# Kernel tuning notes

Measured on AMD Instinct MI355X. Metric: run time of the kernel, lower is better.

## Reference

```python
import jax, jax.numpy as jnp
import numpy as np

T, B, D = 256, 64, 512


def setup_inputs() -> dict:
    key = jax.random.key(0)
    ks = jax.random.split(key, 9)
    s = 1.0 / np.sqrt(D)  # torch Linear default init scale (uniform), use scaled normal
    return {
        "x": jax.random.normal(ks[0], (T, B, D), dtype=jnp.float32),
        "y": jax.random.normal(ks[1], (T, B, D), dtype=jnp.float32),
        "Wr": jax.random.normal(ks[2], (D, D), dtype=jnp.float32) * s,
        "Ur": jax.random.normal(ks[3], (D, D), dtype=jnp.float32) * s,
        "Wz": jax.random.normal(ks[4], (D, D), dtype=jnp.float32) * s,
        "Uz": jax.random.normal(ks[5], (D, D), dtype=jnp.float32) * s,
        "Wg": jax.random.normal(ks[6], (D, D), dtype=jnp.float32) * s,
        "Ug": jax.random.normal(ks[7], (D, D), dtype=jnp.float32) * s,
        "bg": jnp.full((D,), 2.0, dtype=jnp.float32),
    }


def reference(x, y, Wr, Ur, Wz, Uz, Wg, Ug, bg):
    # GTrXL gating unit. torch Linear(y) == y @ W.T
    r = jax.nn.sigmoid(jnp.einsum("tbd,ed->tbe", y, Wr) + jnp.einsum("tbd,ed->tbe", x, Ur))
    z = jax.nn.sigmoid(jnp.einsum("tbd,ed->tbe", y, Wz) + jnp.einsum("tbd,ed->tbe", x, Uz) - bg)
    h = jnp.tanh(jnp.einsum("tbd,ed->tbe", y, Wg) + jnp.einsum("tbd,ed->tbe", r * x, Ug))
    g = (1.0 - z) * x + z * h  # (T, B, D)
    return g
```

## Files before the change

kernel.cpp:

```cpp
#include <hip/hip_runtime.h>
#include <stdint.h>

typedef unsigned short u16;
typedef __attribute__((ext_vector_type(8))) __bf16 bf16x8;
typedef __attribute__((ext_vector_type(4))) float f32x4;

#define Tn 256
#define Bn 64
#define Dn 512
#define Mn (Tn * Bn)


__device__ __forceinline__ u16 f2bf(float f) {
  unsigned u = __float_as_uint(f);
  u += 0x7fffu + ((u >> 16) & 1u);
  return (u16)(u >> 16);
}

__device__ __forceinline__ float bf2f(u16 b) {
  return __uint_as_float(((unsigned)b) << 16);
}

__device__ __forceinline__ void async16(const u16* g, u16* l) {
  __builtin_amdgcn_global_load_lds(
      (const __attribute__((address_space(1))) unsigned int*)g,
      (__attribute__((address_space(3))) unsigned int*)l, 16, 0, 0);
}

__device__ __forceinline__ float sigmoidf_(float v) {
  return 1.f / (1.f + __expf(-v));
}

__global__ void cast_all(const float* __restrict__ y, const float* __restrict__ x,
                         const float* w0, const float* w1, const float* w2,
                         const float* w3, const float* w4, const float* w5,
                         u16* __restrict__ yb, u16* __restrict__ xb,
                         u16* __restrict__ wb) {
  int b = blockIdx.x;
  const float* src;
  u16* dst;
  if (b < 8192) {
    src = y; dst = yb;
  } else if (b < 16384) {
    src = x; dst = xb; b -= 8192;
  } else {
    b -= 16384;
    const int wi = b >> 8;
    b &= 255;
    src = wi == 0 ? w0 : wi == 1 ? w1 : wi == 2 ? w2 : wi == 3 ? w3 : wi == 4 ? w4 : w5;
    dst = wb + wi * 262144;
  }
  const int i4 = b * 256 + (int)threadIdx.x;
  float4 v = ((const float4*)src)[i4];
  ushort4 o;
  o.x = f2bf(v.x); o.y = f2bf(v.y); o.z = f2bf(v.z); o.w = f2bf(v.w);
  ((ushort4*)dst)[i4] = o;
}

__global__ __launch_bounds__(256, 2) void gemm_rzg(
    const u16* __restrict__ yb, const u16* __restrict__ xb,
    const u16* __restrict__ wb,
    const float* __restrict__ xf, const float* __restrict__ bg,
    u16* __restrict__ rxb, u16* __restrict__ zb, float* __restrict__ gacc) {
  __shared__ u16 sY[128 * 64];
  __shared__ u16 sX[128 * 64];
  __shared__ u16 sW[5 * 64 * 64];

  const int tid = threadIdx.x;
  const int lane = tid & 63;
  const int wave = tid >> 6;
  const int waveM = wave >> 1, waveN = wave & 1;
  const int nb = blockIdx.x & 7, mb = blockIdx.x >> 3;
  const int rowStart = mb * 128, colStart = nb * 64;
  const int rbase = tid >> 3;
  const int cbase = (tid & 7) * 8;
  const int wbyte = (tid & 192) * 16;
  const int lm = lane & 15, quad = lane >> 4;

  f32x4 accR[4][2] = {};
  f32x4 accZ[4][2] = {};
  f32x4 accG[4][2] = {};

  for (int k0 = 0; k0 < Dn; k0 += 64) {
#pragma unroll
    for (int s = 0; s < 4; ++s) {
      async16(yb + (size_t)(rowStart + s * 32 + rbase) * Dn + k0 + cbase,
              (u16*)((char*)sY + s * 4096 + wbyte));
      async16(xb + (size_t)(rowStart + s * 32 + rbase) * Dn + k0 + cbase,
              (u16*)((char*)sX + s * 4096 + wbyte));
    }
#pragma unroll
    for (int w = 0; w < 5; ++w)
#pragma unroll
      for (int s = 0; s < 2; ++s)
        async16(wb + (size_t)w * 262144 +
                    (size_t)(colStart + s * 32 + rbase) * Dn + k0 + cbase,
                (u16*)((char*)sW + w * 8192 + s * 4096 + wbyte));
    __syncthreads();

#pragma unroll
    for (int kk = 0; kk < 2; ++kk) {
      bf16x8 ay[4], ax[4], bw[5][2];
#pragma unroll
      for (int i = 0; i < 4; ++i) {
        const int off = (waveM * 64 + i * 16 + lm) * 64 + kk * 32 + quad * 8;
        ay[i] = *(const bf16x8*)(sY + off);
        ax[i] = *(const bf16x8*)(sX + off);
      }
#pragma unroll
      for (int w = 0; w < 5; ++w)
#pragma unroll
        for (int j = 0; j < 2; ++j)
          bw[w][j] = *(const bf16x8*)(sW + w * 4096 +
                                      (waveN * 32 + j * 16 + lm) * 64 + kk * 32 + quad * 8);
#pragma unroll
      for (int i = 0; i < 4; ++i)
#pragma unroll
        for (int j = 0; j < 2; ++j) {
          accR[i][j] = __builtin_amdgcn_mfma_f32_16x16x32_bf16(ay[i], bw[0][j], accR[i][j], 0, 0, 0);
          accR[i][j] = __builtin_amdgcn_mfma_f32_16x16x32_bf16(ax[i], bw[1][j], accR[i][j], 0, 0, 0);
          accZ[i][j] = __builtin_amdgcn_mfma_f32_16x16x32_bf16(ay[i], bw[2][j], accZ[i][j], 0, 0, 0);
          accZ[i][j] = __builtin_amdgcn_mfma_f32_16x16x32_bf16(ax[i], bw[3][j], accZ[i][j], 0, 0, 0);
          accG[i][j] = __builtin_amdgcn_mfma_f32_16x16x32_bf16(ay[i], bw[4][j], accG[i][j], 0, 0, 0);
        }
    }
    __syncthreads();
  }

#pragma unroll
  for (int j = 0; j < 2; ++j) {
    const int e = colStart + waveN * 32 + j * 16 + lm;
    const float bgv = bg[e];
#pragma unroll
    for (int i = 0; i < 4; ++i) {
      const int m0 = rowStart + waveM * 64 + i * 16 + quad * 4;
#pragma unroll
      for (int rg = 0; rg < 4; ++rg) {
        const size_t idx = (size_t)(m0 + rg) * Dn + e;
        const float r = sigmoidf_(accR[i][j][rg]);
        rxb[idx] = f2bf(r * xf[idx]);
        zb[idx] = f2bf(sigmoidf_(accZ[i][j][rg] - bgv));
        gacc[idx] = accG[i][j][rg];
      }
    }
  }
}

__global__ __launch_bounds__(256, 2) void gemm_final(
    const u16* __restrict__ rxb, const u16* __restrict__ ug,
    const u16* __restrict__ zb, const float* __restrict__ xf,
    float* __restrict__ out ) {
  __shared__ u16 sA[128 * 64];
  __shared__ u16 sW[64 * 64];

  const int tid = threadIdx.x;
  const int lane = tid & 63;
  const int wave = tid >> 6;
  const int waveM = wave >> 1, waveN = wave & 1;
  const int nb = blockIdx.x & 7, mb = blockIdx.x >> 3;
  const int rowStart = mb * 128, colStart = nb * 64;
  const int rbase = tid >> 3;
  const int cbase = (tid & 7) * 8;
  const int wbyte = (tid & 192) * 16;
  const int lm = lane & 15, quad = lane >> 4;

  f32x4 acc[4][2] = {};

  for (int k0 = 0; k0 < Dn; k0 += 64) {
#pragma unroll
    for (int s = 0; s < 4; ++s)
      async16(rxb + (size_t)(rowStart + s * 32 + rbase) * Dn + k0 + cbase,
              (u16*)((char*)sA + s * 4096 + wbyte));
#pragma unroll
    for (int s = 0; s < 2; ++s)
      async16(ug + (size_t)(colStart + s * 32 + rbase) * Dn + k0 + cbase,
              (u16*)((char*)sW + s * 4096 + wbyte));
    __syncthreads();

#pragma unroll
    for (int kk = 0; kk < 2; ++kk) {
      bf16x8 aa[4], bw[2];
#pragma unroll
      for (int i = 0; i < 4; ++i)
        aa[i] = *(const bf16x8*)(sA + (waveM * 64 + i * 16 + lm) * 64 + kk * 32 + quad * 8);
#pragma unroll
      for (int j = 0; j < 2; ++j)
        bw[j] = *(const bf16x8*)(sW + (waveN * 32 + j * 16 + lm) * 64 + kk * 32 + quad * 8);
#pragma unroll
      for (int i = 0; i < 4; ++i)
#pragma unroll
        for (int j = 0; j < 2; ++j)
          acc[i][j] = __builtin_amdgcn_mfma_f32_16x16x32_bf16(aa[i], bw[j], acc[i][j], 0, 0, 0);
    }
    __syncthreads();
  }

#pragma unroll
  for (int j = 0; j < 2; ++j) {
    const int e = colStart + waveN * 32 + j * 16 + lm;
#pragma unroll
    for (int i = 0; i < 4; ++i) {
      const int m0 = rowStart + waveM * 64 + i * 16 + quad * 4;
#pragma unroll
      for (int rg = 0; rg < 4; ++rg) {
        const size_t idx = (size_t)(m0 + rg) * Dn + e;
        const float pre = out[idx] + acc[i][j][rg];
        const float ex = __expf(-2.f * pre);
        const float h = (1.f - ex) / (1.f + ex);
        const float z = bf2f(zb[idx]);
        const float xv = xf[idx];
        out[idx] = (1.f - z) * xv + z * h;
      }
    }
  }
}

extern "C" void kernel_launch(void* const* d_in, const int* in_sizes, int n_in,
                              void* d_out, int out_size, void* d_ws, size_t ws_size,
                              hipStream_t stream) {
  const float* x  = (const float*)d_in[0];
  const float* y  = (const float*)d_in[1];
  const float* Wr = (const float*)d_in[2];
  const float* Ur = (const float*)d_in[3];
  const float* Wz = (const float*)d_in[4];
  const float* Uz = (const float*)d_in[5];
  const float* Wg = (const float*)d_in[6];
  const float* Ug = (const float*)d_in[7];
  const float* bg = (const float*)d_in[8];
  float* out = (float*)d_out;

  char* ws = (char*)d_ws;
  u16* yb  = (u16*)(ws);
  u16* xb  = (u16*)(ws + 16777216);
  u16* rxb = (u16*)(ws + 2 * 16777216);
  u16* wb  = (u16*)(ws + 3 * 16777216);
  u16* zb  = (u16*)(ws + 3 * 16777216 + 3145728);

  cast_all<<<17920, 256, 0, stream>>>(y, x, Wr, Ur, Wz, Uz, Wg, Ug, yb, xb, wb);
  gemm_rzg<<<1024, 256, 0, stream>>>(yb, xb, wb, x, bg, rxb, zb, out);
  gemm_final<<<1024, 256, 0, stream>>>(rxb, wb + (size_t)5 * 262144, zb, x, out);
}
```

Baseline: 228.7 us.

## Move Wg GEMM into final kernel as concatenated-K GEMM, read bf16 x

The y·Wg product moves out of the first GEMM kernel. It is now computed in the final kernel, which loops over a concatenated K dimension: first y with Wg, then r*x with Ug. This removes the fp32 intermediate written to the output buffer and read back, so global memory traffic drops. Both epilogues now read the bf16 copy of x instead of the fp32 input, which cuts traffic further but uses a rounded x in the gate blend and in r*x.

Measured after the change: 224.3 us. Within noise of the previous version (-1.9%).

```diff
diff --git a/kernel.cpp b/kernel.cpp
--- a/kernel.cpp
+++ b/kernel.cpp
@@ -5,10 +5,8 @@
 typedef __attribute__((ext_vector_type(8))) __bf16 bf16x8;
 typedef __attribute__((ext_vector_type(4))) float f32x4;
 
-#define Tn 256
-#define Bn 64
 #define Dn 512
-#define Mn (Tn * Bn)
+#define Mn 16384
 
 
 __device__ __forceinline__ u16 f2bf(float f) {
@@ -57,14 +55,14 @@
   ((ushort4*)dst)[i4] = o;
 }
 
-__global__ __launch_bounds__(256, 2) void gemm_rzg(
+__global__ __launch_bounds__(256, 2) void gemm_rz(
     const u16* __restrict__ yb, const u16* __restrict__ xb,
     const u16* __restrict__ wb,
-    const float* __restrict__ xf, const float* __restrict__ bg,
-    u16* __restrict__ rxb, u16* __restrict__ zb, float* __restrict__ gacc) {
+    const float* __restrict__ bg,
+    u16* __restrict__ rxb, u16* __restrict__ zb) {
   __shared__ u16 sY[128 * 64];
   __shared__ u16 sX[128 * 64];
-  __shared__ u16 sW[5 * 64 * 64];
+  __shared__ u16 sW[4 * 64 * 64];
 
   const int tid = threadIdx.x;
   const int lane = tid & 63;
@@ -79,7 +77,6 @@
 
   f32x4 accR[4][2] = {};
   f32x4 accZ[4][2] = {};
-  f32x4 accG[4][2] = {};
 
   for (int k0 = 0; k0 < Dn; k0 += 64) {
 #pragma unroll
@@ -90,7 +87,7 @@
               (u16*)((char*)sX + s * 4096 + wbyte));
     }
 #pragma unroll
-    for (int w = 0; w < 5; ++w)
+    for (int w = 0; w < 4; ++w)
 #pragma unroll
       for (int s = 0; s < 2; ++s)
         async16(wb + (size_t)w * 262144 +
@@ -100,7 +97,7 @@
 
 #pragma unroll
     for (int kk = 0; kk < 2; ++kk) {
-      bf16x8 ay[4], ax[4], bw[5][2];
+      bf16x8 ay[4], ax[4], bw[4][2];
 #pragma unroll
       for (int i = 0; i < 4; ++i) {
         const int off = (waveM * 64 + i * 16 + lm) * 64 + kk * 32 + quad * 8;
@@ -108,7 +105,7 @@
         ax[i] = *(const bf16x8*)(sX + off);
       }
 #pragma unroll
-      for (int w = 0; w < 5; ++w)
+      for (int w = 0; w < 4; ++w)
 #pragma unroll
         for (int j = 0; j < 2; ++j)
           bw[w][j] = *(const bf16x8*)(sW + w * 4096 +
@@ -121,7 +118,6 @@
           accR[i][j] = __builtin_amdgcn_mfma_f32_16x16x32_bf16(ax[i], bw[1][j], accR[i][j], 0, 0, 0);
           accZ[i][j] = __builtin_amdgcn_mfma_f32_16x16x32_bf16(ay[i], bw[2][j], accZ[i][j], 0, 0, 0);
           accZ[i][j] = __builtin_amdgcn_mfma_f32_16x16x32_bf16(ax[i], bw[3][j], accZ[i][j], 0, 0, 0);
-          accG[i][j] = __builtin_amdgcn_mfma_f32_16x16x32_bf16(ay[i], bw[4][j], accG[i][j], 0, 0, 0);
         }
     }
     __syncthreads();
@@ -138,18 +134,18 @@
       for (int rg = 0; rg < 4; ++rg) {
         const size_t idx = (size_t)(m0 + rg) * Dn + e;
         const float r = sigmoidf_(accR[i][j][rg]);
-        rxb[idx] = f2bf(r * xf[idx]);
+        rxb[idx] = f2bf(r * bf2f(xb[idx]));
         zb[idx] = f2bf(sigmoidf_(accZ[i][j][rg] - bgv));
-        gacc[idx] = accG[i][j][rg];
       }
     }
   }
 }
 
-__global__ __launch_bounds__(256, 2) void gemm_final(
-    const u16* __restrict__ rxb, const u16* __restrict__ ug,
-    const u16* __restrict__ zb, const float* __restrict__ xf,
-    float* __restrict__ out ) {
+__global__ __launch_bounds__(256, 2) void gemm_gu(
+    const u16* __restrict__ yb, const u16* __restrict__ rxb,
+    const u16* __restrict__ wg,
+    const u16* __restrict__ zb, const u16* __restrict__ xb,
+    float* __restrict__ out) {
   __shared__ u16 sA[128 * 64];
   __shared__ u16 sW[64 * 64];
 
@@ -166,14 +162,18 @@
 
   f32x4 acc[4][2] = {};
 
-  for (int k0 = 0; k0 < Dn; k0 += 64) {
+  for (int kq = 0; kq < 16; ++kq) {
+    const int half = kq >> 3;
+    const int k0 = (kq & 7) * 64;
+    const u16* abase = half ? rxb : yb;
+    const u16* wbase = wg + (size_t)half * 262144;
 #pragma unroll
     for (int s = 0; s < 4; ++s)
-      async16(rxb + (size_t)(rowStart + s * 32 + rbase) * Dn + k0 + cbase,
+      async16(abase + (size_t)(rowStart + s * 32 + rbase) * Dn + k0 + cbase,
               (u16*)((char*)sA + s * 4096 + wbyte));
 #pragma unroll
     for (int s = 0; s < 2; ++s)
-      async16(ug + (size_t)(colStart + s * 32 + rbase) * Dn + k0 + cbase,
+      async16(wbase + (size_t)(colStart + s * 32 + rbase) * Dn + k0 + cbase,
               (u16*)((char*)sW + s * 4096 + wbyte));
     __syncthreads();
 
@@ -204,11 +204,11 @@
 #pragma unroll
       for (int rg = 0; rg < 4; ++rg) {
         const size_t idx = (size_t)(m0 + rg) * Dn + e;
-        const float pre = out[idx] + acc[i][j][rg];
+        const float pre = acc[i][j][rg];
         const float ex = __expf(-2.f * pre);
         const float h = (1.f - ex) / (1.f + ex);
         const float z = bf2f(zb[idx]);
-        const float xv = xf[idx];
+        const float xv = bf2f(xb[idx]);
         out[idx] = (1.f - z) * xv + z * h;
       }
     }
@@ -237,6 +237,6 @@
   u16* zb  = (u16*)(ws + 3 * 16777216 + 3145728);
 
   cast_all<<<17920, 256, 0, stream>>>(y, x, Wr, Ur, Wz, Uz, Wg, Ug, yb, xb, wb);
-  gemm_rzg<<<1024, 256, 0, stream>>>(yb, xb, wb, x, bg, rxb, zb, out);
-  gemm_final<<<1024, 256, 0, stream>>>(rxb, wb + (size_t)5 * 262144, zb, x, out);
-}
+  gemm_rz<<<1024, 256, 0, stream>>>(yb, xb, wb, bg, rxb, zb);
+  gemm_gu<<<1024, 256, 0, stream>>>(yb, rxb, wb + (size_t)4 * 262144, zb, xb, out);
+}
```
